# Performance work log

Measured on AMD Instinct MI355X. Metric: run time of the kernel, lower is better.

Reference implementation:

```python
import jax, jax.numpy as jnp
import numpy as np

N, H, W, K = 16, 512, 512, 1
V, F = 6890, 13776

def setup_inputs() -> dict:
    key = jax.random.key(0)
    k1, k2, k3, k4 = jax.random.split(key, 4)
    pix_to_face = jax.random.randint(k1, (N, H, W, K), 0, N * F, dtype=jnp.int64 if jax.config.jax_enable_x64 else jnp.int32)
    bary_coords = jax.random.uniform(k2, (N, H, W, K, 3), dtype=jnp.float32)
    faces = jax.random.randint(k3, (F, 3), 0, V, dtype=jnp.int32)
    verts_scene_flow = jax.random.normal(k4, (N, V, 3), dtype=jnp.float32)
    return {"pix_to_face": pix_to_face, "bary_coords": bary_coords, "faces": faces, "verts_scene_flow": verts_scene_flow}

def gen_mesh_grid(Hh, Ww):
    h_grid = jnp.linspace(-1.0, 1.0, Hh)  # along H
    v_grid = jnp.linspace(-1.0, 1.0, Ww)  # along W
    gy = jnp.broadcast_to(h_grid[:, None], (Hh, Ww))
    gx = jnp.broadcast_to(v_grid[None, :], (Hh, Ww))
    grid = jnp.stack([gx, gy, jnp.zeros((Hh, Ww), jnp.float32)], axis=-1)  # [H,W,3]
    return grid

def reference(pix_to_face, bary_coords, faces, verts_scene_flow):
    n, v, _ = verts_scene_flow.shape
    f = faces.shape[0]
    # padded_to_packed: [N,V,3] -> [N*V,3]
    verts_packed = verts_scene_flow.reshape(n * v, 3)
    # faces_packed: offset each mesh's face indices by i*V -> [N*F,3]
    offsets = (jnp.arange(n, dtype=faces.dtype) * v)[:, None, None]
    faces_packed = (faces[None, :, :] + offsets).reshape(n * f, 3)
    # faces_flow: gather verts per face -> [N*F,3,3]
    faces_flow = verts_packed[faces_packed]
    # interpolate_face_attributes: mask invalid pixels (pix_to_face < 0)
    mask = pix_to_face >= 0
    safe_idx = jnp.where(mask, pix_to_face, 0)
    attrs = faces_flow[safe_idx]  # [N,H,W,K,3,3]
    pixel_flow = jnp.einsum('nhwkv,nhwkvc->nhwkc', bary_coords, attrs)
    pixel_flow = jnp.where(mask[..., None], pixel_flow, 0.0)
    # squeeze K and add precomputed mesh grid
    hh, ww = pix_to_face.shape[1], pix_to_face.shape[2]
    grid = gen_mesh_grid(hh, ww)
    return pixel_flow[:, :, :, 0, :] + grid[None]
```

## Files before the change

### kernel.cpp

```cpp
#include <hip/hip_runtime.h>

#define N_  16
#define H_  512
#define W_  512
#define F_  13776
#define V_  6890
#define NF_ (N_ * F_)

typedef float ntf4 __attribute__((ext_vector_type(4)));
typedef int   nti4 __attribute__((ext_vector_type(4)));
typedef unsigned int uint_t;
typedef struct { int x, y, z; } iface3;

__global__ __launch_bounds__(256) void prep_faces_kernel(
    const int*   __restrict__ faces,
    const float* __restrict__ verts,
    nti4*        __restrict__ table)
{
    const int gf = blockIdx.x * 256 + threadIdx.x;
    const int mesh = gf / F_;
    const int loc  = gf - mesh * F_;
    const int vb   = mesh * V_;
    const iface3 f = *(const iface3*)(faces + loc * 3);
    const float3 v0 = *(const float3*)(verts + (f.x + vb) * 3);
    const float3 v1 = *(const float3*)(verts + (f.y + vb) * 3);
    const float3 v2 = *(const float3*)(verts + (f.z + vb) * 3);

    float vals[9] = {v0.x, v0.y, v0.z, v1.x, v1.y, v1.z, v2.x, v2.y, v2.z};
    float m = 0.0f;
    #pragma unroll
    for (int i = 0; i < 9; ++i) m = fmaxf(m, fabsf(vals[i]));
    int e  = (int)(__float_as_uint(m) >> 23) - 127;
    int be = e + 20;
    be = be < 0 ? 0 : (be > 31 ? 31 : be);
    const float senc = __uint_as_float((uint_t)(158 - be) << 23);

    uint_t fq[9];
    #pragma unroll
    for (int i = 0; i < 9; ++i) {
        int qi = (int)rintf(vals[i] * senc);
        qi = qi > 4095 ? 4095 : (qi < -4096 ? -4096 : qi);
        fq[i] = (uint_t)qi & 0x1FFFu;
    }
    nti4 r;
    r.x = (int)(fq[0] | (fq[1] << 13) | ((fq[8] & 0x3Fu) << 26));
    r.y = (int)(fq[2] | (fq[3] << 13) | (((fq[8] >> 6) & 0x3Fu) << 26));
    r.z = (int)(fq[4] | (fq[5] << 13) | (((fq[8] >> 12) & 1u) << 26)
                      | ((uint_t)be << 27));
    r.w = (int)(fq[6] | (fq[7] << 13));
    table[gf] = r;
}

__device__ __forceinline__ void decode_quad(
    const nti4* q, const bool* valid, const float w[4][3], int p0,
    ntf4& o0, ntf4& o1, ntf4& o2)
{
    const float step = 2.0f / 511.0f;
    float r[4][3];
    #pragma unroll
    for (int i = 0; i < 4; ++i) {
        const uint_t d0 = (uint_t)q[i].x, d1 = (uint_t)q[i].y,
                     d2 = (uint_t)q[i].z, d3 = (uint_t)q[i].w;
        const int q0 = ((int)(d0 << 19)) >> 19;
        const int q1 = ((int)(d0 <<  6)) >> 19;
        const int q2 = ((int)(d1 << 19)) >> 19;
        const int q3 = ((int)(d1 <<  6)) >> 19;
        const int q4 = ((int)(d2 << 19)) >> 19;
        const int q5 = ((int)(d2 <<  6)) >> 19;
        const int q6 = ((int)(d3 << 19)) >> 19;
        const int q7 = ((int)(d3 <<  6)) >> 19;
        const uint_t u8 = (d0 >> 26) | ((d1 >> 26) << 6) | (((d2 >> 26) & 1u) << 12);
        const int q8 = ((int)(u8 << 19)) >> 19;
        const float scale = __uint_as_float(((d2 >> 27) + 96u) << 23);

        float ox = (w[i][0] * (float)q0 + w[i][1] * (float)q3 + w[i][2] * (float)q6) * scale;
        float oy = (w[i][0] * (float)q1 + w[i][1] * (float)q4 + w[i][2] * (float)q7) * scale;
        float oz = (w[i][0] * (float)q2 + w[i][1] * (float)q5 + w[i][2] * (float)q8) * scale;
        if (!valid[i]) { ox = 0.f; oy = 0.f; oz = 0.f; }
        const int p = p0 + i;
        r[i][0] = ox + (float)(p & (W_ - 1)) * step - 1.0f;
        r[i][1] = oy + (float)((p >> 9) & (H_ - 1)) * step - 1.0f;
        r[i][2] = oz;
    }
    o0.x = r[0][0]; o0.y = r[0][1]; o0.z = r[0][2]; o0.w = r[1][0];
    o1.x = r[1][1]; o1.y = r[1][2]; o1.z = r[2][0]; o1.w = r[2][1];
    o2.x = r[2][2]; o2.y = r[3][0]; o2.z = r[3][1]; o2.w = r[3][2];
}

__global__ __launch_bounds__(256, 4) void OpticalFlowShader_kernel(
    const nti4* __restrict__ ptf,
    const ntf4* __restrict__ bary,
    const nti4* __restrict__ table,
    ntf4*       __restrict__ out)
{
    __shared__ ntf4 lds[1536];

    const int tid   = threadIdx.x;
    const int tA    = blockIdx.x * 512 + tid;
    const int tB    = tA + 256;
    const int fbase = blockIdx.x * 1536;

    const nti4 pfA = __builtin_nontemporal_load(&ptf[tA]);
    const nti4 pfB = __builtin_nontemporal_load(&ptf[tB]);

    ntf4 c[6];
    #pragma unroll
    for (int k = 0; k < 6; ++k)
        c[k] = __builtin_nontemporal_load(&bary[fbase + tid + 256 * k]);

    const int fidA[4] = {pfA.x, pfA.y, pfA.z, pfA.w};
    const int fidB[4] = {pfB.x, pfB.y, pfB.z, pfB.w};
    nti4 qA[4], qB[4];
    bool vA[4], vB[4];
    #pragma unroll
    for (int i = 0; i < 4; ++i) {
        vA[i] = fidA[i] >= 0;
        qA[i] = table[vA[i] ? fidA[i] : 0];
    }
    #pragma unroll
    for (int i = 0; i < 4; ++i) {
        vB[i] = fidB[i] >= 0;
        qB[i] = table[vB[i] ? fidB[i] : 0];
    }

    #pragma unroll
    for (int k = 0; k < 6; ++k) lds[tid + 256 * k] = c[k];
    __syncthreads();
    const ntf4 a0 = lds[tid * 3 + 0];
    const ntf4 a1 = lds[tid * 3 + 1];
    const ntf4 a2 = lds[tid * 3 + 2];
    const ntf4 e0 = lds[tid * 3 + 768];
    const ntf4 e1 = lds[tid * 3 + 769];
    const ntf4 e2 = lds[tid * 3 + 770];
    __syncthreads();

    const float wA[4][3] = {
        {a0.x, a0.y, a0.z}, {a0.w, a1.x, a1.y},
        {a1.z, a1.w, a2.x}, {a2.y, a2.z, a2.w},
    };
    const float wB[4][3] = {
        {e0.x, e0.y, e0.z}, {e0.w, e1.x, e1.y},
        {e1.z, e1.w, e2.x}, {e2.y, e2.z, e2.w},
    };

    ntf4 o0, o1, o2;
    decode_quad(qA, vA, wA, 4 * tA, o0, o1, o2);
    lds[tid * 3 + 0] = o0;
    lds[tid * 3 + 1] = o1;
    lds[tid * 3 + 2] = o2;
    decode_quad(qB, vB, wB, 4 * tB, o0, o1, o2);
    lds[tid * 3 + 768] = o0;
    lds[tid * 3 + 769] = o1;
    lds[tid * 3 + 770] = o2;
    __syncthreads();

    #pragma unroll
    for (int k = 0; k < 6; ++k)
        __builtin_nontemporal_store(lds[tid + 256 * k], &out[fbase + tid + 256 * k]);
}

__global__ __launch_bounds__(256) void OpticalFlowShader_fallback(
    const nti4*  __restrict__ ptf,
    const ntf4*  __restrict__ bary,
    const int*   __restrict__ faces,
    const float* __restrict__ verts,
    ntf4*        __restrict__ out)
{
    const int t = blockIdx.x * 256 + threadIdx.x;
    const nti4 pf = __builtin_nontemporal_load(&ptf[t]);
    const ntf4 b0 = __builtin_nontemporal_load(&bary[t * 3 + 0]);
    const ntf4 b1 = __builtin_nontemporal_load(&bary[t * 3 + 1]);
    const ntf4 b2 = __builtin_nontemporal_load(&bary[t * 3 + 2]);
    const int fid[4] = {pf.x, pf.y, pf.z, pf.w};
    const float w[4][3] = {
        {b0.x, b0.y, b0.z}, {b0.w, b1.x, b1.y},
        {b1.z, b1.w, b2.x}, {b2.y, b2.z, b2.w},
    };
    int base[4][3]; bool valid[4];
    #pragma unroll
    for (int i = 0; i < 4; ++i) {
        valid[i] = fid[i] >= 0;
        const int sf = valid[i] ? fid[i] : 0;
        const int mesh = sf / F_;
        const int loc  = sf - mesh * F_;
        const int vb   = mesh * V_;
        const iface3 f = *(const iface3*)(faces + loc * 3);
        base[i][0] = (f.x + vb) * 3;
        base[i][1] = (f.y + vb) * 3;
        base[i][2] = (f.z + vb) * 3;
    }
    float3 v[4][3];
    #pragma unroll
    for (int i = 0; i < 4; ++i)
        #pragma unroll
        for (int j = 0; j < 3; ++j)
            v[i][j] = *(const float3*)(verts + base[i][j]);
    const float step = 2.0f / 511.0f;
    const int p0 = 4 * t;
    float r[4][3];
    #pragma unroll
    for (int i = 0; i < 4; ++i) {
        float ox = w[i][0]*v[i][0].x + w[i][1]*v[i][1].x + w[i][2]*v[i][2].x;
        float oy = w[i][0]*v[i][0].y + w[i][1]*v[i][1].y + w[i][2]*v[i][2].y;
        float oz = w[i][0]*v[i][0].z + w[i][1]*v[i][1].z + w[i][2]*v[i][2].z;
        if (!valid[i]) { ox = 0.f; oy = 0.f; oz = 0.f; }
        const int p = p0 + i;
        r[i][0] = ox + (float)(p & (W_ - 1)) * step - 1.0f;
        r[i][1] = oy + (float)((p >> 9) & (H_ - 1)) * step - 1.0f;
        r[i][2] = oz;
    }
    ntf4 o0; o0.x = r[0][0]; o0.y = r[0][1]; o0.z = r[0][2]; o0.w = r[1][0];
    ntf4 o1; o1.x = r[1][1]; o1.y = r[1][2]; o1.z = r[2][0]; o1.w = r[2][1];
    ntf4 o2; o2.x = r[2][2]; o2.y = r[3][0]; o2.z = r[3][1]; o2.w = r[3][2];
    __builtin_nontemporal_store(o0, &out[t * 3 + 0]);
    __builtin_nontemporal_store(o1, &out[t * 3 + 1]);
    __builtin_nontemporal_store(o2, &out[t * 3 + 2]);
}

extern "C" void kernel_launch(void* const* d_in, const int* in_sizes, int n_in,
                              void* d_out, int out_size, void* d_ws, size_t ws_size,
                              hipStream_t stream) {
    const nti4*  ptf   = (const nti4*)d_in[0];
    const ntf4*  bary  = (const ntf4*)d_in[1];
    const int*   faces = (const int*)d_in[2];
    const float* verts = (const float*)d_in[3];
    ntf4*        out   = (ntf4*)d_out;

    const int quads  = (N_ * H_ * W_) / 4;
    const size_t table_bytes = (size_t)NF_ * 16;
    if (ws_size >= table_bytes) {
        nti4* table = (nti4*)d_ws;
        prep_faces_kernel<<<NF_ / 256, 256, 0, stream>>>(faces, verts, table);
        OpticalFlowShader_kernel<<<quads / 512, 256, 0, stream>>>(ptf, bary, table, out);
    } else {
        OpticalFlowShader_fallback<<<quads / 256, 256, 0, stream>>>(ptf, bary, faces, verts, out);
    }
}
```

Before: 140.2 us.

## Make LDS transpose wave-private to drop block barriers, raise occupancy hint

Each wavefront now owns a private 384-entry slice of shared memory for the AoS/SoA transpose of barycentrics and outputs. The block-wide __syncthreads are replaced with s_waitcnt lgkmcnt(0), and launch bounds go from 4 to 6 blocks per CU. This removes cross-wave barrier stalls so waves can run their load/compute/store phases independently. It relies on wave-level LDS ordering and gives the compiler a tighter register budget.

After: 140.0 us. No clear change (-0.2%).

```diff
diff --git a/kernel.cpp b/kernel.cpp
--- a/kernel.cpp
+++ b/kernel.cpp
@@ -87,7 +87,7 @@
     o2.x = r[2][2]; o2.y = r[3][0]; o2.z = r[3][1]; o2.w = r[3][2];
 }
 
-__global__ __launch_bounds__(256, 4) void OpticalFlowShader_kernel(
+__global__ __launch_bounds__(256, 6) void OpticalFlowShader_kernel(
     const nti4* __restrict__ ptf,
     const ntf4* __restrict__ bary,
     const nti4* __restrict__ table,
@@ -95,9 +95,11 @@
 {
     __shared__ ntf4 lds[1536];
 
-    const int tid   = threadIdx.x;
-    const int tA    = blockIdx.x * 512 + tid;
-    const int tB    = tA + 256;
+    const int lane  = threadIdx.x & 63;
+    const int wv    = threadIdx.x >> 6;
+    const int wbase = wv * 384;
+    const int tA    = blockIdx.x * 512 + wv * 128 + lane;
+    const int tB    = tA + 64;
     const int fbase = blockIdx.x * 1536;
 
     const nti4 pfA = __builtin_nontemporal_load(&ptf[tA]);
@@ -106,7 +108,7 @@
     ntf4 c[6];
     #pragma unroll
     for (int k = 0; k < 6; ++k)
-        c[k] = __builtin_nontemporal_load(&bary[fbase + tid + 256 * k]);
+        c[k] = __builtin_nontemporal_load(&bary[fbase + wbase + lane + 64 * k]);
 
     const int fidA[4] = {pfA.x, pfA.y, pfA.z, pfA.w};
     const int fidB[4] = {pfB.x, pfB.y, pfB.z, pfB.w};
@@ -124,15 +126,15 @@
     }
 
     #pragma unroll
-    for (int k = 0; k < 6; ++k) lds[tid + 256 * k] = c[k];
-    __syncthreads();
-    const ntf4 a0 = lds[tid * 3 + 0];
-    const ntf4 a1 = lds[tid * 3 + 1];
-    const ntf4 a2 = lds[tid * 3 + 2];
-    const ntf4 e0 = lds[tid * 3 + 768];
-    const ntf4 e1 = lds[tid * 3 + 769];
-    const ntf4 e2 = lds[tid * 3 + 770];
-    __syncthreads();
+    for (int k = 0; k < 6; ++k) lds[wbase + lane + 64 * k] = c[k];
+    asm volatile("s_waitcnt lgkmcnt(0)" ::: "memory");
+    const ntf4 a0 = lds[wbase + lane * 3 + 0];
+    const ntf4 a1 = lds[wbase + lane * 3 + 1];
+    const ntf4 a2 = lds[wbase + lane * 3 + 2];
+    const ntf4 e0 = lds[wbase + 192 + lane * 3 + 0];
+    const ntf4 e1 = lds[wbase + 192 + lane * 3 + 1];
+    const ntf4 e2 = lds[wbase + 192 + lane * 3 + 2];
+    asm volatile("s_waitcnt lgkmcnt(0)" ::: "memory");
 
     const float wA[4][3] = {
         {a0.x, a0.y, a0.z}, {a0.w, a1.x, a1.y},
@@ -145,18 +147,19 @@
 
     ntf4 o0, o1, o2;
     decode_quad(qA, vA, wA, 4 * tA, o0, o1, o2);
-    lds[tid * 3 + 0] = o0;
-    lds[tid * 3 + 1] = o1;
-    lds[tid * 3 + 2] = o2;
+    lds[wbase + lane * 3 + 0] = o0;
+    lds[wbase + lane * 3 + 1] = o1;
+    lds[wbase + lane * 3 + 2] = o2;
     decode_quad(qB, vB, wB, 4 * tB, o0, o1, o2);
-    lds[tid * 3 + 768] = o0;
-    lds[tid * 3 + 769] = o1;
-    lds[tid * 3 + 770] = o2;
-    __syncthreads();
+    lds[wbase + 192 + lane * 3 + 0] = o0;
+    lds[wbase + 192 + lane * 3 + 1] = o1;
+    lds[wbase + 192 + lane * 3 + 2] = o2;
+    asm volatile("s_waitcnt lgkmcnt(0)" ::: "memory");
 
     #pragma unroll
     for (int k = 0; k < 6; ++k)
-        __builtin_nontemporal_store(lds[tid + 256 * k], &out[fbase + tid + 256 * k]);
+        __builtin_nontemporal_store(lds[wbase + lane + 64 * k],
+                                    &out[fbase + wbase + lane + 64 * k]);
 }
 
 __global__ __launch_bounds__(256) void OpticalFlowShader_fallback(
```
